# Kernel tuning notes

Hardware: AMD Instinct MI355X
Metric: run time of the kernel (lower is better)

## Reference

```python
import jax, jax.numpy as jnp
import numpy as np

EPS = 0.1        # entropic regularization (self.eps)
THRESH = 0.1     # convergence threshold on sum|u - u1| (self.thresh)
MAX_ITER = 100   # self.max_iter
K = 8            # num_neighbors in get_mask_matrix


def setup_inputs() -> dict:
    key = jax.random.key(0)
    k1, k2, k3 = jax.random.split(key, 3)
    B, N, M = 8, 3000, 3000
    mu = jax.random.uniform(k1, (B, N), dtype=jnp.float32)
    mu = mu / mu.sum(-1, keepdims=True)
    nu = jax.random.uniform(k2, (B, M), dtype=jnp.float32)
    nu = nu / nu.sum(-1, keepdims=True)
    C = jax.random.uniform(k3, (B, N, M), dtype=jnp.float32)
    return {"mu": mu, "nu": nu, "C": C}


def _knn_mask(C, k=K):
    # get_mask_matrix: k smallest per row (dim=1) + k largest per column (dim=0)
    B, N, M = C.shape
    _, ir = jax.lax.top_k(-C, k)                       # [B,N,k] smallest along cols
    row_mask = jnp.zeros(C.shape, C.dtype).at[
        jnp.arange(B)[:, None, None], jnp.arange(N)[None, :, None], ir].set(1.0)
    _, ic = jax.lax.top_k(jnp.swapaxes(C, -1, -2), k)  # [B,M,k] largest along rows
    col_mask = jnp.zeros(C.shape, C.dtype).at[
        jnp.arange(B)[:, None, None], ic, jnp.arange(M)[None, :, None]].set(1.0)
    return ((row_mask + col_mask) > 0).astype(C.dtype)


def _sinkhorn(mu, nu, C, A):
    # log-domain Sinkhorn of get_dist, vectorized over batch with per-sample early stop
    B = mu.shape[0]
    log_mu = jnp.log(mu + 1e-8)
    log_nu = jnp.log(nu + 1e-8)

    def exp_M(u, v):
        return A * jnp.exp((-C + u[:, :, None] + v[:, None, :]) / EPS)

    def step(carry, _):
        u, v, done = carry
        u_new = EPS * (log_mu - jnp.log(1e-8 + exp_M(u, v).sum(-1))) + u
        v_new = EPS * (log_nu - jnp.log(1e-8 + exp_M(u_new, v).sum(-2))) + v
        err = jnp.abs(u_new - u).sum(-1)               # [B]
        u_out = jnp.where(done[:, None], u, u_new)
        v_out = jnp.where(done[:, None], v, v_new)
        done = done | (err < THRESH)
        return (u_out, v_out, done), None

    init = (jnp.zeros_like(mu), jnp.zeros_like(nu), jnp.zeros((B,), dtype=bool))
    (u, v, _), _ = jax.lax.scan(step, init, None, length=MAX_ITER)
    pi = exp_M(u, v)
    return jnp.sum(pi * C, axis=(-2, -1))              # [B]


def reference(mu, nu, C):
    # get_cost_matrix: row-wise L2 normalization (F.normalize p=2 dim=1)
    Cn = C / jnp.maximum(jnp.linalg.norm(C, axis=-1, keepdims=True), 1e-12)
    A = _knn_mask(Cn)
    Cm = A * Cn                                        # C = A.to_dense() * C
    cost = _sinkhorn(mu, nu, Cm, A)
    return cost.mean()                                 # gwd / batch
```

## Files before the change

kernel.cpp:

```cpp
#include <hip/hip_runtime.h>
#include <cfloat>

typedef unsigned long long ull;

constexpr int NB = 8, NN = 3000, NM = 3000, KK = 8;
constexpr int CAP = 48;
constexpr float SCALE   = 14.426950408889634f;
constexpr float UNSCALE = 0.06931471805599453f;
constexpr float THRESH  = 0.1f;
constexpr unsigned DUMMY_PAT = 0x7f7f7f7fu;
constexpr int NCH = 32;

constexpr int BPB  = 8;
constexpr int NBLK = NB * BPB;
constexpr int TPB  = 512;
constexpr int RPB  = NN / BPB;

#if __has_builtin(__builtin_amdgcn_exp2f)
#define FEXP2(x) __builtin_amdgcn_exp2f(x)
#else
#define FEXP2(x) exp2f(x)
#endif
#if __has_builtin(__builtin_amdgcn_logf)
#define FLOG2(x) __builtin_amdgcn_logf(x)
#else
#define FLOG2(x) __log2f(x)
#endif

__device__ __forceinline__ ull aload64(const ull* p) {
  return __hip_atomic_load(p, __ATOMIC_RELAXED, __HIP_MEMORY_SCOPE_AGENT);
}
__device__ __forceinline__ void astore64(ull* p, ull x) {
  __hip_atomic_store(p, x, __ATOMIC_RELAXED, __HIP_MEMORY_SCOPE_AGENT);
}

__device__ __forceinline__ void pull_tagged(const ull* __restrict__ src, int tag,
                                            float* __restrict__ dst, int lane) {
  const int nfull = RPB - 5 * 64;
  unsigned pend = (lane < nfull) ? 0x3Fu : 0x1Fu;
  {
    ull x0 = aload64(&src[lane]);
    ull x1 = aload64(&src[lane + 64]);
    ull x2 = aload64(&src[lane + 128]);
    ull x3 = aload64(&src[lane + 192]);
    ull x4 = aload64(&src[lane + 256]);
    ull x5 = (lane < nfull) ? aload64(&src[lane + 320]) : 0;
    if ((int)(x0 >> 32) == tag) { dst[lane]       = __uint_as_float((unsigned)x0); pend &= ~1u;  }
    if ((int)(x1 >> 32) == tag) { dst[lane + 64]  = __uint_as_float((unsigned)x1); pend &= ~2u;  }
    if ((int)(x2 >> 32) == tag) { dst[lane + 128] = __uint_as_float((unsigned)x2); pend &= ~4u;  }
    if ((int)(x3 >> 32) == tag) { dst[lane + 192] = __uint_as_float((unsigned)x3); pend &= ~8u;  }
    if ((int)(x4 >> 32) == tag) { dst[lane + 256] = __uint_as_float((unsigned)x4); pend &= ~16u; }
    if ((lane < nfull) && (int)(x5 >> 32) == tag) { dst[lane + 320] = __uint_as_float((unsigned)x5); pend &= ~32u; }
  }
  while (pend) {
    __builtin_amdgcn_s_sleep(1);
#pragma unroll
    for (int j = 0; j < 6; ++j) {
      if (!((pend >> j) & 1u)) continue;
      ull x = aload64(&src[lane + 64 * j]);
      if ((int)(x >> 32) == tag) {
        dst[lane + 64 * j] = __uint_as_float((unsigned)x);
        pend &= ~(1u << j);
      }
    }
  }
}

__global__ __launch_bounds__(256) void k_rowprep(const float* __restrict__ C,
                                                 float* __restrict__ invnorms,
                                                 int2* __restrict__ rowsel) {
  const int bn = blockIdx.x * 8 + (threadIdx.x >> 5);
  const int l  = threadIdx.x & 31;
  const float4* row4 = reinterpret_cast<const float4*>(C + (size_t)bn * NM);

  float tv[8]; int ti[8];
#pragma unroll
  for (int q = 0; q < 8; ++q) { tv[q] = FLT_MAX; ti[q] = 0x7fffffff; }
  float sq = 0.f;
  for (int c = 0; c < 24; ++c) {
    int i = l + 32 * c;
    if (i < NM / 4) {
      float4 f = row4[i];
      sq += f.x * f.x + f.y * f.y + f.z * f.z + f.w * f.w;
      float e[4] = { f.x, f.y, f.z, f.w };
#pragma unroll
      for (int j = 0; j < 4; ++j) {
        float v = e[j];
        if (v < tv[7]) {
          int idx = 4 * i + j;
          int pos = 8;
#pragma unroll
          for (int q = 7; q >= 0; --q) if (v < tv[q]) pos = q;
#pragma unroll
          for (int q = 7; q >= 1; --q) if (q > pos) { tv[q] = tv[q-1]; ti[q] = ti[q-1]; }
#pragma unroll
          for (int q = 0; q < 8; ++q) if (q == pos) { tv[q] = v; ti[q] = idx; }
        }
      }
    }
  }
#pragma unroll
  for (int o = 16; o; o >>= 1) sq += __shfl_down(sq, o, 32);

#pragma unroll
  for (int msk = 1; msk <= 16; msk <<= 1) {
    float pv[8]; int pi[8];
#pragma unroll
    for (int q = 0; q < 8; ++q) { pv[q] = __shfl_xor(tv[q], msk); pi[q] = __shfl_xor(ti[q], msk); }
    float mv[8]; int mi[8];
#pragma unroll
    for (int q = 0; q < 8; ++q) {
      float av = tv[q], bv = pv[7 - q];
      int   ai = ti[q], bi = pi[7 - q];
      bool ta = (av < bv) || (av == bv && ai < bi);
      mv[q] = ta ? av : bv; mi[q] = ta ? ai : bi;
    }
    auto ce = [&](int i, int j) {
      bool sw = (mv[i] > mv[j]) || (mv[i] == mv[j] && mi[i] > mi[j]);
      float fv = sw ? mv[j] : mv[i], gv = sw ? mv[i] : mv[j];
      int   fi = sw ? mi[j] : mi[i], gi = sw ? mi[i] : mi[j];
      mv[i] = fv; mv[j] = gv; mi[i] = fi; mi[j] = gi;
    };
    ce(0,4); ce(1,5); ce(2,6); ce(3,7);
    ce(0,2); ce(1,3); ce(4,6); ce(5,7);
    ce(0,1); ce(2,3); ce(4,5); ce(6,7);
#pragma unroll
    for (int q = 0; q < 8; ++q) { tv[q] = mv[q]; ti[q] = mi[q]; }
  }

  if (l == 0) {
#pragma unroll
    for (int q = 0; q < 8; ++q)
      rowsel[(size_t)bn * KK + q] = make_int2(ti[q], __float_as_int(tv[q]));
    float nm = sqrtf(sq);
    invnorms[bn] = 1.0f / fmaxf(nm, 1e-12f);
  }
}

__global__ __launch_bounds__(256) void k_coltop1(const float* __restrict__ C,
                                                 const float* __restrict__ invnorms,
                                                 ull* __restrict__ partial) {
  const int b = blockIdx.z, rc = blockIdx.y, cg = blockIdx.x;
  const int tid = threadIdx.x;
  const int w = tid >> 6, l = tid & 63;
  const int g4 = cg * 64 + l;
  const int chunk = rc * 4 + w;

  ull tv[4][8];
#pragma unroll
  for (int j = 0; j < 4; ++j)
#pragma unroll
    for (int q = 0; q < 8; ++q) tv[j][q] = 0;

  if (g4 < NM / 4) {
    const int base_r = rc * 375;
    const int r0 = base_r + w * 94;
    const int r1 = min(base_r + 375, r0 + 94);
    const float4* base = reinterpret_cast<const float4*>(
        C + (size_t)b * NN * NM) + g4;
    const float* ivn = invnorms + (size_t)b * NN;
    for (int n = r0; n < r1; ++n) {
      float4 f = base[(size_t)n * (NM / 4)];
      float iv = ivn[n];
      float e[4] = { f.x * iv, f.y * iv, f.z * iv, f.w * iv };
      ull lo = (ull)(unsigned)~n;
#pragma unroll
      for (int j = 0; j < 4; ++j) {
        ull key = ((ull)__float_as_uint(e[j]) << 32) | lo;
        if (key > tv[j][7]) {
          int pos = 8;
#pragma unroll
          for (int q = 7; q >= 0; --q) if (key > tv[j][q]) pos = q;
#pragma unroll
          for (int q = 7; q >= 1; --q) if (q > pos) tv[j][q] = tv[j][q-1];
#pragma unroll
          for (int q = 0; q < 8; ++q) if (q == pos) tv[j][q] = key;
        }
      }
    }
    ull* dst = partial + (((size_t)b * NCH + chunk) * NM + (size_t)4 * g4) * 8;
#pragma unroll
    for (int j = 0; j < 4; ++j)
#pragma unroll
      for (int q = 0; q < 8; ++q) dst[j * 8 + q] = tv[j][q];
  }
}

__global__ __launch_bounds__(256) void k_coltop2(const ull* __restrict__ partial,
                                                 int2* __restrict__ colsel) {
  int t = blockIdx.x * 256 + threadIdx.x;
  if (t >= NB * NM) return;
  int b = t / NM, m = t % NM;
  ull top[8];
#pragma unroll
  for (int q = 0; q < 8; ++q) top[q] = 0;
  for (int c = 0; c < NCH; ++c) {
    const ull* src = partial + (((size_t)b * NCH + c) * NM + m) * 8;
    ull buf[8];
#pragma unroll
    for (int q = 0; q < 8; ++q) buf[q] = src[q];
    for (int q = 0; q < 8; ++q) {
      ull key = buf[q];
      if (key <= top[7]) break;
      int pos = 8;
#pragma unroll
      for (int z = 7; z >= 0; --z) if (key > top[z]) pos = z;
#pragma unroll
      for (int z = 7; z >= 1; --z) if (z > pos) top[z] = top[z-1];
#pragma unroll
      for (int z = 0; z < 8; ++z) if (z == pos) top[z] = key;
    }
  }
#pragma unroll
  for (int q = 0; q < 8; ++q)
    colsel[(size_t)t * KK + q] =
        make_int2((int)~(unsigned)top[q], (int)(top[q] >> 32));
}

__global__ __launch_bounds__(256) void k_fill(const float* __restrict__ invnorms,
    const int2* __restrict__ rowsel, const int2* __restrict__ colsel,
    int* r_cnt, int* c_cnt, int2* __restrict__ r_pk, int2* __restrict__ c_pk) {
  int t = blockIdx.x * 256 + threadIdx.x;
  if (t >= NB * NN * KK) return;
  int k = t % KK; int bn = t / KK;
  int b = bn / NN; int n = bn % NN;
  float inv_bn = invnorms[bn];
  int2 rs = rowsel[t];
  int2 cs = colsel[t];
  {
    float v2 = __int_as_float(rs.y) * inv_bn * SCALE;
    r_pk[(size_t)bn * CAP + k] = make_int2(rs.x, __float_as_int(v2));
  }
  {
    float v2 = __int_as_float(cs.y) * SCALE;
    c_pk[(size_t)bn * CAP + k] = make_int2(cs.x, __float_as_int(v2));
  }
  int m = n;
  {
    int n3 = cs.x;
    const int2* rl = rowsel + ((size_t)b * NN + n3) * KK;
    bool dup = false;
#pragma unroll
    for (int q = 0; q < KK; ++q) dup |= (rl[q].x == m);
    if (!dup) {
      int slot = 8 + atomicAdd(&r_cnt[(size_t)b * NN + n3], 1);
      if (slot < CAP) {
        float v2 = __int_as_float(cs.y) * SCALE;
        r_pk[((size_t)b * NN + n3) * CAP + slot] = make_int2(m, __float_as_int(v2));
      }
    }
  }
  {
    int mm = rs.x;
    const int2* cl = colsel + ((size_t)b * NM + mm) * KK;
    bool dup = false;
#pragma unroll
    for (int q = 0; q < KK; ++q) dup |= (cl[q].x == n);
    if (!dup) {
      int slot = 8 + atomicAdd(&c_cnt[(size_t)b * NM + mm], 1);
      if (slot < CAP) {
        float v2 = __int_as_float(rs.y) * inv_bn * SCALE;
        c_pk[((size_t)b * NM + mm) * CAP + slot] = make_int2(n, __float_as_int(v2));
      }
    }
  }
}

__global__ __launch_bounds__(TPB, 1) void k_sink_coop(
    const float* __restrict__ mu, const float* __restrict__ nu,
    const int2* __restrict__ r_pk, const int2* __restrict__ c_pk,
    ull* __restrict__ Upub, ull* __restrict__ Vpub,
    ull* errW, float* __restrict__ costpart) {
  const int blk = blockIdx.x;
  const int b = blk % NB, slice = blk / NB;
  const int tid = threadIdx.x;
  const int w = tid >> 6, lane = tid & 63;
  const int r = slice * RPB + tid;
  const bool has_r = (tid < RPB);

  float rval[CAP], cval[CAP];
  unsigned ridx[CAP / 2], cidx[CAP / 2];
  float u = 0.f, vv = 0.f, lmu = 0.f, lnu = 0.f;
  if (has_r) {
    const int2* rp = r_pk + ((size_t)b * NN + r) * CAP;
    const int2* cp = c_pk + ((size_t)b * NM + r) * CAP;
#pragma unroll
    for (int i = 0; i < CAP; i += 2) {
      int2 e0 = rp[i], e1 = rp[i + 1];
      rval[i] = __int_as_float(e0.y); rval[i + 1] = __int_as_float(e1.y);
      unsigned i0 = min((unsigned)e0.x & 0xFFFFu, (unsigned)(NN - 1));
      unsigned i1 = min((unsigned)e1.x & 0xFFFFu, (unsigned)(NN - 1));
      ridx[i / 2] = i0 | (i1 << 16);
      int2 f0 = cp[i], f1 = cp[i + 1];
      cval[i] = __int_as_float(f0.y); cval[i + 1] = __int_as_float(f1.y);
      unsigned j0 = min((unsigned)f0.x & 0xFFFFu, (unsigned)(NN - 1));
      unsigned j1 = min((unsigned)f1.x & 0xFFFFu, (unsigned)(NN - 1));
      cidx[i / 2] = j0 | (j1 << 16);
    }
    lmu = FLOG2(mu[(size_t)b * NN + r] + 1e-8f);
    lnu = FLOG2(nu[(size_t)b * NM + r] + 1e-8f);
  }

  __shared__ float XL[NN];
  __shared__ float sred[TPB / 64];
  __shared__ float errl[BPB];
  int itf = 0;
  bool done = false;

  for (int it = 0; it < 100; ++it) {
    if (it == 0) {
      for (int i = tid; i < NN; i += TPB) XL[i] = 0.f;
    } else {
      if (has_r) XL[r] = vv;
      if (w != slice) {
        const ull* src = Vpub + (size_t)((it - 1) & 1) * (NB * NN)
                       + (size_t)b * NN + (size_t)w * RPB;
        pull_tagged(src, it, XL + w * RPB, lane);
      }
    }
    __syncthreads();

    float errp = 0.f;
    if (has_r) {
      float s = 0.f;
#pragma unroll
      for (int i = 0; i < CAP; ++i) {
        int ix = (ridx[i >> 1] >> ((i & 1) * 16)) & 0xFFFF;
        s += FEXP2(u + XL[ix] - rval[i]);
      }
      float un = lmu - FLOG2(1e-8f + s) + u;
      errp = fabsf(un - u);
      u = un;
      astore64(&Upub[(size_t)(it & 1) * (NB * NN) + (size_t)b * NN + r],
               ((ull)(unsigned)(it + 1) << 32) | __float_as_uint(u));
    }
#pragma unroll
    for (int o = 32; o; o >>= 1) errp += __shfl_down(errp, o);
    if (lane == 0) sred[w] = errp;
    __syncthreads();
    if (tid == 0) {
      float e = sred[0] + sred[1] + sred[2] + sred[3]
              + sred[4] + sred[5] + sred[6] + sred[7];
      astore64(&errW[(size_t)((it & 1) * NB + b) * BPB * 16 + slice * 16],
               ((ull)(unsigned)(it + 1) << 32) | __float_as_uint(e));
      errl[slice] = e;
    }

    if (has_r) XL[r] = u;
    if (w != slice) {
      const ull* src = Upub + (size_t)(it & 1) * (NB * NN)
                     + (size_t)b * NN + (size_t)w * RPB;
      pull_tagged(src, it + 1, XL + w * RPB, lane);
      if (lane == 0) {
        const ull* ep = errW + (size_t)((it & 1) * NB + b) * BPB * 16 + w * 16;
        ull x = aload64(ep);
        while ((int)(x >> 32) != it + 1) { __builtin_amdgcn_s_sleep(1); x = aload64(ep); }
        errl[w] = __uint_as_float((unsigned)x);
      }
    }
    __syncthreads();

    float errtot = errl[0] + errl[1] + errl[2] + errl[3]
                 + errl[4] + errl[5] + errl[6] + errl[7];
    done = (errtot * UNSCALE < THRESH);
    if (has_r) {
      float s = 0.f;
#pragma unroll
      for (int i = 0; i < CAP; ++i) {
        int ix = (cidx[i >> 1] >> ((i & 1) * 16)) & 0xFFFF;
        s += FEXP2(vv + XL[ix] - cval[i]);
      }
      vv = lnu - FLOG2(1e-8f + s) + vv;
      astore64(&Vpub[(size_t)(it & 1) * (NB * NN) + (size_t)b * NN + r],
               ((ull)(unsigned)(it + 1) << 32) | __float_as_uint(vv));
    }
    __syncthreads();
    itf = it;
    if (done) break;
  }

  if (has_r) XL[r] = vv;
  if (w != slice) {
    const ull* src = Vpub + (size_t)(itf & 1) * (NB * NN)
                   + (size_t)b * NN + (size_t)w * RPB;
    pull_tagged(src, itf + 1, XL + w * RPB, lane);
  }
  __syncthreads();
  float cs = 0.f;
  if (has_r) {
#pragma unroll
    for (int i = 0; i < CAP; ++i) {
      int ix = (ridx[i >> 1] >> ((i & 1) * 16)) & 0xFFFF;
      float val = rval[i];
      cs += FEXP2(u + XL[ix] - val) * val;
    }
  }
#pragma unroll
  for (int o = 32; o; o >>= 1) cs += __shfl_down(cs, o);
  if (lane == 0) sred[w] = cs;
  __syncthreads();
  if (tid == 0)
    costpart[b * BPB + slice] = sred[0] + sred[1] + sred[2] + sred[3]
                              + sred[4] + sred[5] + sred[6] + sred[7];
}

__global__ void k_final2(const float* __restrict__ costpart, float* __restrict__ out) {
  if (threadIdx.x == 0 && blockIdx.x == 0) {
    float tot = 0.f;
    for (int b = 0; b < NB; ++b) {
      float cb = 0.f;
      for (int s = 0; s < BPB; ++s) cb += costpart[b * BPB + s];
      tot += cb * UNSCALE;
    }
    out[0] = tot * (1.0f / NB);
  }
}

extern "C" void kernel_launch(void* const* d_in, const int* in_sizes, int n_in,
                              void* d_out, int out_size, void* d_ws, size_t ws_size,
                              hipStream_t stream) {
  const float* mu = (const float*)d_in[0];
  const float* nu = (const float*)d_in[1];
  const float* C  = (const float*)d_in[2];
  float* out = (float*)d_out;

  char* ws = (char*)d_ws;
  size_t off = 0;
  auto alloc = [&](size_t bytes) {
    void* p = ws + off;
    off += (bytes + 255) & ~(size_t)255;
    return p;
  };
  float* invnorms = (float*)alloc(sizeof(float) * NB * NN);
  int2*  rowsel   = (int2*) alloc(sizeof(int2)  * NB * NN * KK);
  int2*  colsel   = (int2*) alloc(sizeof(int2)  * NB * NM * KK);
  ull*   partial  = (ull*)  alloc(sizeof(ull)   * NB * NCH * NM * 8);
  int2*  r_pk     = (int2*) alloc(sizeof(int2)  * NB * NN * CAP);
  int2*  c_pk     = (int2*) alloc(sizeof(int2)  * NB * NM * CAP);
  ull*   Upub     = (ull*)  alloc(sizeof(ull)   * 2 * NB * NN);
  ull*   Vpub     = (ull*)  alloc(sizeof(ull)   * 2 * NB * NM);
  ull*   errW     = (ull*)  alloc(sizeof(ull)   * 2 * NB * BPB * 16);
  int*   r_cnt    = (int*)  alloc(sizeof(int)   * NB * NN);
  int*   c_cnt    = (int*)  alloc(sizeof(int)   * NB * NM);
  float* costpart = (float*)alloc(sizeof(float) * NB * BPB);
  (void)ws_size; (void)in_sizes; (void)n_in; (void)out_size;

  hipMemsetD32Async((hipDeviceptr_t)r_pk, (int)DUMMY_PAT,
                    (size_t)2 * NB * NN * CAP * 2, stream);
  size_t span = (size_t)((char*)costpart - (char*)Upub)
              + ((sizeof(float) * NB * BPB + 255) & ~(size_t)255);
  hipMemsetAsync(Upub, 0, span, stream);

  hipLaunchKernelGGL(k_rowprep, dim3(NB * NN / 8), dim3(256), 0, stream,
                     C, invnorms, rowsel);
  hipLaunchKernelGGL(k_coltop1, dim3(12, NCH / 4, NB), dim3(256), 0, stream,
                     C, invnorms, partial);
  hipLaunchKernelGGL(k_coltop2, dim3((NB * NM + 255) / 256), dim3(256), 0, stream,
                     partial, colsel);
  int nthreads = NB * NN * KK;
  hipLaunchKernelGGL(k_fill, dim3((nthreads + 255) / 256), dim3(256), 0, stream,
                     invnorms, rowsel, colsel, r_cnt, c_cnt, r_pk, c_pk);

  void* args[] = { (void*)&mu, (void*)&nu, (void*)&r_pk, (void*)&c_pk,
                   (void*)&Upub, (void*)&Vpub, (void*)&errW, (void*)&costpart };
  hipLaunchCooperativeKernel((const void*)k_sink_coop, dim3(NBLK), dim3(TPB),
                             args, 0, stream);

  hipLaunchKernelGGL(k_final2, dim3(1), dim3(64), 0, stream, costpart, out);
}
```

Measured before the change: 831.9 us.

## Halve blocks per batch in cooperative Sinkhorn and split remote pulls into quarters

The cooperative Sinkhorn kernel now uses 4 blocks of 1024 threads per batch sample instead of 8 blocks of 512, so each block owns 750 rows and there are fewer cross-block peers to exchange potentials and error values with. Remote slices are pulled by 12 waves, each loading a quarter slice, and the error-word poll is issued before the slice pull. The goal is to cut inter-block spin-wait latency on each iteration. The trade-off is half as many blocks (32) on the GPU and more register pressure per block. k_coltop2 also moves to 64-thread blocks to spread work across more CUs.

```diff
diff --git a/kernel.cpp b/kernel.cpp
--- a/kernel.cpp
+++ b/kernel.cpp
@@ -11,10 +11,11 @@
 constexpr unsigned DUMMY_PAT = 0x7f7f7f7fu;
 constexpr int NCH = 32;
 
-constexpr int BPB  = 8;
+constexpr int BPB  = 4;
 constexpr int NBLK = NB * BPB;
-constexpr int TPB  = 512;
+constexpr int TPB  = 1024;
 constexpr int RPB  = NN / BPB;
+constexpr int QLEN = 188;
 
 #if __has_builtin(__builtin_amdgcn_exp2f)
 #define FEXP2(x) __builtin_amdgcn_exp2f(x)
@@ -34,32 +35,30 @@
   __hip_atomic_store(p, x, __ATOMIC_RELAXED, __HIP_MEMORY_SCOPE_AGENT);
 }
 
-__device__ __forceinline__ void pull_tagged(const ull* __restrict__ src, int tag,
-                                            float* __restrict__ dst, int lane) {
-  const int nfull = RPB - 5 * 64;
-  unsigned pend = (lane < nfull) ? 0x3Fu : 0x1Fu;
-  {
-    ull x0 = aload64(&src[lane]);
-    ull x1 = aload64(&src[lane + 64]);
-    ull x2 = aload64(&src[lane + 128]);
-    ull x3 = aload64(&src[lane + 192]);
-    ull x4 = aload64(&src[lane + 256]);
-    ull x5 = (lane < nfull) ? aload64(&src[lane + 320]) : 0;
-    if ((int)(x0 >> 32) == tag) { dst[lane]       = __uint_as_float((unsigned)x0); pend &= ~1u;  }
-    if ((int)(x1 >> 32) == tag) { dst[lane + 64]  = __uint_as_float((unsigned)x1); pend &= ~2u;  }
-    if ((int)(x2 >> 32) == tag) { dst[lane + 128] = __uint_as_float((unsigned)x2); pend &= ~4u;  }
-    if ((int)(x3 >> 32) == tag) { dst[lane + 192] = __uint_as_float((unsigned)x3); pend &= ~8u;  }
-    if ((int)(x4 >> 32) == tag) { dst[lane + 256] = __uint_as_float((unsigned)x4); pend &= ~16u; }
-    if ((lane < nfull) && (int)(x5 >> 32) == tag) { dst[lane + 320] = __uint_as_float((unsigned)x5); pend &= ~32u; }
-  }
+__device__ __forceinline__ void pull_quarter(const ull* __restrict__ src, int tag,
+                                             float* __restrict__ dst,
+                                             int lane, int q) {
+  const int start = q * QLEN;
+  const int len = min(QLEN, RPB - start);
+  unsigned pend = 0;
+  if (lane < len)       pend |= 1u;
+  if (lane + 64 < len)  pend |= 2u;
+  if (lane + 128 < len) pend |= 4u;
+  ull x0 = 0, x1 = 0, x2 = 0;
+  if (pend & 1u) x0 = aload64(&src[start + lane]);
+  if (pend & 2u) x1 = aload64(&src[start + lane + 64]);
+  if (pend & 4u) x2 = aload64(&src[start + lane + 128]);
+  if ((pend & 1u) && (int)(x0 >> 32) == tag) { dst[start + lane]       = __uint_as_float((unsigned)x0); pend &= ~1u; }
+  if ((pend & 2u) && (int)(x1 >> 32) == tag) { dst[start + lane + 64]  = __uint_as_float((unsigned)x1); pend &= ~2u; }
+  if ((pend & 4u) && (int)(x2 >> 32) == tag) { dst[start + lane + 128] = __uint_as_float((unsigned)x2); pend &= ~4u; }
   while (pend) {
     __builtin_amdgcn_s_sleep(1);
 #pragma unroll
-    for (int j = 0; j < 6; ++j) {
+    for (int j = 0; j < 3; ++j) {
       if (!((pend >> j) & 1u)) continue;
-      ull x = aload64(&src[lane + 64 * j]);
+      ull x = aload64(&src[start + lane + 64 * j]);
       if ((int)(x >> 32) == tag) {
-        dst[lane + 64 * j] = __uint_as_float((unsigned)x);
+        dst[start + lane + 64 * j] = __uint_as_float((unsigned)x);
         pend &= ~(1u << j);
       }
     }
@@ -186,9 +185,9 @@
   }
 }
 
-__global__ __launch_bounds__(256) void k_coltop2(const ull* __restrict__ partial,
-                                                 int2* __restrict__ colsel) {
-  int t = blockIdx.x * 256 + threadIdx.x;
+__global__ __launch_bounds__(64) void k_coltop2(const ull* __restrict__ partial,
+                                                int2* __restrict__ colsel) {
+  int t = blockIdx.x * 64 + threadIdx.x;
   if (t >= NB * NM) return;
   int b = t / NM, m = t % NM;
   ull top[8];
@@ -277,6 +276,10 @@
   const int w = tid >> 6, lane = tid & 63;
   const int r = slice * RPB + tid;
   const bool has_r = (tid < RPB);
+  const bool puller = (w < 12);
+  const int p_idx = w >> 2;
+  const int prod = p_idx + (p_idx >= slice ? 1 : 0);
+  const int quar = w & 3;
 
   float rval[CAP], cval[CAP];
   unsigned ridx[CAP / 2], cidx[CAP / 2];
@@ -312,10 +315,10 @@
       for (int i = tid; i < NN; i += TPB) XL[i] = 0.f;
     } else {
       if (has_r) XL[r] = vv;
-      if (w != slice) {
+      if (puller) {
         const ull* src = Vpub + (size_t)((it - 1) & 1) * (NB * NN)
-                       + (size_t)b * NN + (size_t)w * RPB;
-        pull_tagged(src, it, XL + w * RPB, lane);
+                       + (size_t)b * NN + (size_t)prod * RPB;
+        pull_quarter(src, it, XL + prod * RPB, lane, quar);
       }
     }
     __syncthreads();
@@ -339,29 +342,31 @@
     if (lane == 0) sred[w] = errp;
     __syncthreads();
     if (tid == 0) {
-      float e = sred[0] + sred[1] + sred[2] + sred[3]
-              + sred[4] + sred[5] + sred[6] + sred[7];
+      float e = 0.f;
+#pragma unroll
+      for (int k = 0; k < 16; ++k) e += sred[k];
       astore64(&errW[(size_t)((it & 1) * NB + b) * BPB * 16 + slice * 16],
                ((ull)(unsigned)(it + 1) << 32) | __float_as_uint(e));
       errl[slice] = e;
     }
 
     if (has_r) XL[r] = u;
-    if (w != slice) {
+    if (puller) {
+      const bool eneed = (quar == 0) && (lane == 0);
+      const ull* ep = errW + (size_t)((it & 1) * NB + b) * BPB * 16 + prod * 16;
+      ull ex = 0;
+      if (eneed) ex = aload64(ep);
       const ull* src = Upub + (size_t)(it & 1) * (NB * NN)
-                     + (size_t)b * NN + (size_t)w * RPB;
-      pull_tagged(src, it + 1, XL + w * RPB, lane);
-      if (lane == 0) {
-        const ull* ep = errW + (size_t)((it & 1) * NB + b) * BPB * 16 + w * 16;
-        ull x = aload64(ep);
-        while ((int)(x >> 32) != it + 1) { __builtin_amdgcn_s_sleep(1); x = aload64(ep); }
-        errl[w] = __uint_as_float((unsigned)x);
+                     + (size_t)b * NN + (size_t)prod * RPB;
+      pull_quarter(src, it + 1, XL + prod * RPB, lane, quar);
+      if (eneed) {
+        while ((int)(ex >> 32) != it + 1) { __builtin_amdgcn_s_sleep(1); ex = aload64(ep); }
+        errl[prod] = __uint_as_float((unsigned)ex);
       }
     }
     __syncthreads();
 
-    float errtot = errl[0] + errl[1] + errl[2] + errl[3]
-                 + errl[4] + errl[5] + errl[6] + errl[7];
+    float errtot = errl[0] + errl[1] + errl[2] + errl[3];
     done = (errtot * UNSCALE < THRESH);
     if (has_r) {
       float s = 0.f;
@@ -380,10 +385,10 @@
   }
 
   if (has_r) XL[r] = vv;
-  if (w != slice) {
+  if (puller) {
     const ull* src = Vpub + (size_t)(itf & 1) * (NB * NN)
-                   + (size_t)b * NN + (size_t)w * RPB;
-    pull_tagged(src, itf + 1, XL + w * RPB, lane);
+                   + (size_t)b * NN + (size_t)prod * RPB;
+    pull_quarter(src, itf + 1, XL + prod * RPB, lane, quar);
   }
   __syncthreads();
   float cs = 0.f;
@@ -399,9 +404,12 @@
   for (int o = 32; o; o >>= 1) cs += __shfl_down(cs, o);
   if (lane == 0) sred[w] = cs;
   __syncthreads();
-  if (tid == 0)
-    costpart[b * BPB + slice] = sred[0] + sred[1] + sred[2] + sred[3]
-                              + sred[4] + sred[5] + sred[6] + sred[7];
+  if (tid == 0) {
+    float tot = 0.f;
+#pragma unroll
+    for (int k = 0; k < 16; ++k) tot += sred[k];
+    costpart[b * BPB + slice] = tot;
+  }
 }
 
 __global__ void k_final2(const float* __restrict__ costpart, float* __restrict__ out) {
@@ -455,7 +463,7 @@
                      C, invnorms, rowsel);
   hipLaunchKernelGGL(k_coltop1, dim3(12, NCH / 4, NB), dim3(256), 0, stream,
                      C, invnorms, partial);
-  hipLaunchKernelGGL(k_coltop2, dim3((NB * NM + 255) / 256), dim3(256), 0, stream,
+  hipLaunchKernelGGL(k_coltop2, dim3((NB * NM + 63) / 64), dim3(64), 0, stream,
                      partial, colsel);
   int nthreads = NB * NN * KK;
   hipLaunchKernelGGL(k_fill, dim3((nthreads + 255) / 256), dim3(256), 0, stream,
```

New measurement: 2.174 ms. 2.61x slower.
